# Performance work log

Measured on AMD Instinct MI355X. Metric: run time of the kernel, lower is better.

## Reference

```python
import jax, jax.numpy as jnp
import numpy as np

# BEV grid constants from init_kwargs (gen_dx_bx)
DX = jnp.array([0.3, 0.3, 20.0], dtype=jnp.float32)          # dx
BX_LO = jnp.array([-54.0, -54.0, -10.0], dtype=jnp.float32)  # bx - dx/2 = lower bound
NXX, NXY, NZ = 360, 360, 1                                    # nx = (360, 360, 1)


def setup_inputs() -> dict:
    key = jax.random.key(0)
    k1, k2, k3 = jax.random.split(key, 3)
    B, D, fH, fW, C = 4, 118, 32, 88, 80
    iH, iW = 256, 704
    x = jax.random.normal(k1, (B, D, fH, fW, C), dtype=jnp.float32)
    # frustum exactly as create_frustum(): (D, fH, fW, 3) with (u, v, depth)
    ds = jnp.arange(1.0, 60.0, 0.5, dtype=jnp.float32)[:, None, None] * jnp.ones((1, fH, fW), jnp.float32)
    xs = jnp.linspace(0.0, iW - 1.0, fW, dtype=jnp.float32)[None, None, :] * jnp.ones((D, fH, 1), jnp.float32)
    ys = jnp.linspace(0.0, iH - 1.0, fH, dtype=jnp.float32)[None, :, None] * jnp.ones((D, 1, fW), jnp.float32)
    frustum = jnp.stack([xs, ys, ds], axis=-1)
    # realistic pinhole intrinsics (well-conditioned for torch.inverse analog)
    fx = 560.0
    K = jnp.array([[fx, 0.0, (iW - 1) / 2.0], [0.0, fx, (iH - 1) / 2.0], [0.0, 0.0, 1.0]], dtype=jnp.float32)
    intrins = jnp.tile(K[None], (B, 1, 1))
    # camera->lidar: cam z -> lidar x, cam x -> -y, cam y -> -z, with small yaw jitter per sample
    Rbase = jnp.array([[0.0, 0.0, 1.0], [-1.0, 0.0, 0.0], [0.0, -1.0, 0.0]], dtype=jnp.float32)
    ang = jax.random.uniform(k2, (B,), minval=-0.2, maxval=0.2, dtype=jnp.float32)
    c, s = jnp.cos(ang), jnp.sin(ang)
    z0, o = jnp.zeros_like(c), jnp.ones_like(c)
    Ryaw = jnp.stack([jnp.stack([c, -s, z0], -1), jnp.stack([s, c, z0], -1), jnp.stack([z0, z0, o], -1)], axis=-2)
    rots = Ryaw @ Rbase[None]
    trans = jax.random.normal(k3, (B, 3), dtype=jnp.float32) * 0.5
    return {"x": x, "camera2lidar_rots": rots, "camera2lidar_trans": trans, "intrins": intrins, "frustum": frustum}


def reference(x, camera2lidar_rots, camera2lidar_trans, intrins, frustum):
    B, D, H, W, C = x.shape
    # --- get_geometry ---
    # unproject pixel (u,v,d) -> camera coords (u*d, v*d, d)
    pts = jnp.concatenate([frustum[..., :2] * frustum[..., 2:3], frustum[..., 2:3]], axis=-1)  # (D,H,W,3)
    combine = camera2lidar_rots @ jnp.linalg.inv(intrins)  # (B,3,3)
    geom = jnp.einsum('bij,dhwj->bdhwi', combine, pts) + camera2lidar_trans[:, None, None, None, :]  # (B,D,H,W,3)
    # --- bev_pool ---
    feats = x.reshape(-1, C)                                      # (Nprime, C)
    # torch .long() truncates toward zero -> numpy-style astype cast matches
    coords = ((geom - BX_LO) / DX).astype(jnp.int32).reshape(-1, 3)  # (Nprime, 3) voxel ix
    Np = feats.shape[0]
    batch_ix = jnp.repeat(jnp.arange(B, dtype=jnp.int32), Np // B)
    nx = jnp.array([NXX, NXY, NZ], dtype=jnp.int32)
    kept = jnp.all((coords >= 0) & (coords < nx), axis=-1)
    # linear voxel index ordered (b, z, x, y); out-of-range points go to a trash segment
    lin = ((batch_ix * NZ + coords[:, 2]) * NXX + coords[:, 0]) * NXY + coords[:, 1]
    nseg = B * NZ * NXX * NXY
    lin = jnp.where(kept, lin, nseg)
    pooled = jax.ops.segment_sum(feats, lin, num_segments=nseg + 1)[:-1]  # (B*Z*X*Y, C)
    out = pooled.reshape(B, NZ, NXX, NXY, C).transpose(0, 1, 4, 2, 3)     # (B, Z, C, X, Y)
    # torch: cat(unbind(dim=2 of (B,C,Z,X,Y)), dim=1) == (B, Z*C, X, Y) with Z-major blocks
    final = out.reshape(B, NZ * C, NXX, NXY)
    return final
```

## Files before the change

kernel.cpp:

```cpp
#include <hip/hip_runtime.h>
#include <hip/hip_bf16.h>

constexpr int B  = 4;
constexpr int D  = 118;
constexpr int FH = 32;
constexpr int FW = 88;
constexpr int C  = 80;
constexpr int NX = 360, NY = 360;
constexpr int XY = NX * NY;
constexpr int OUT_PER_B = C * XY;
constexpr int CELLS = B * XY;
constexpr int RPB = D * FW;
constexpr int CAP = 64;

constexpr int WPB = 16;
constexpr int NWB = (FW + WPB - 1) / WPB;
constexpr int K1_THREADS = WPB * (C / 4);

constexpr size_t CNT_BYTES    = (size_t)CELLS * 4;
constexpr size_t BUCKET_BYTES = (size_t)CELLS * CAP * 2;
constexpr size_t RAYFEAT_OFF  = CNT_BYTES + BUCKET_BYTES;


__global__ __launch_bounds__(K1_THREADS)
void ray_reduce_kernel(const float* __restrict__ x,
                       const float* __restrict__ rots,
                       const float* __restrict__ trans,
                       const float* __restrict__ intr,
                       const float* __restrict__ fr,
                       int* __restrict__ cnt,
                       unsigned short* __restrict__ bucket,
                       float* __restrict__ rayfeat) {
    const int g  = blockIdx.x;
    const int wg = g % NWB;
    const int bd = g / NWB;
    const int d  = bd % D;
    const int b  = bd / D;

    __shared__ int      sCell[WPB];
    __shared__ unsigned sMask[WPB];

    const int tid = threadIdx.x;

    if (tid < WPB) {
        const int w = wg * WPB + tid;
        int cell = -1;
        unsigned zmask = 0;
        if (w < FW) {
            const float* K = intr + b * 9;
            const float* R = rots + b * 9;
            const float i00 = 1.0f / K[0];
            const float i11 = 1.0f / K[4];
            const float i22 = 1.0f / K[8];
            const float i12 = -(K[5] * i22) / K[4];
            const float i01 = -(K[1] * i11) / K[0];
            const float i02 = -(fmaf(K[1], i12, K[2] * i22)) / K[0];
            const float inv[9] = { i00, i01, i02, 0.f, i11, i12, 0.f, 0.f, i22 };
            float cb[9];
            #pragma unroll
            for (int i = 0; i < 3; ++i) {
                #pragma unroll
                for (int j = 0; j < 3; ++j) {
                    float a = R[i * 3 + 0] * inv[0 * 3 + j];
                    a = fmaf(R[i * 3 + 1], inv[1 * 3 + j], a);
                    a = fmaf(R[i * 3 + 2], inv[2 * 3 + j], a);
                    cb[i * 3 + j] = a;
                }
            }
            const float tx = trans[b * 3 + 0];
            const float ty = trans[b * 3 + 1];
            const float tz = trans[b * 3 + 2];

            const float* frd = fr + (size_t)d * FH * FW * 3;
            const float dd = frd[2];
            const float u  = frd[w * 3 + 0];
            const float v0 = frd[1];

            const float p0 = u * dd;
            const float p2 = dd;
            const float p1_0 = v0 * dd;

            const float g0 = fmaf(cb[2], p2, fmaf(cb[1], p1_0, cb[0] * p0)) + tx;
            const float g1 = fmaf(cb[5], p2, fmaf(cb[4], p1_0, cb[3] * p0)) + ty;
            const int c0 = (int)((g0 + 54.0f) / 0.3f);
            const int c1 = (int)((g1 + 54.0f) / 0.3f);

            #pragma unroll
            for (int h = 0; h < FH; ++h) {
                const float vh = frd[h * FW * 3 + 1];
                const float p1h = vh * dd;
                const float g2 = fmaf(cb[8], p2, fmaf(cb[7], p1h, cb[6] * p0)) + tz;
                const int c2 = (int)((g2 + 10.0f) / 20.0f);
                if (c2 == 0) zmask |= (1u << h);
            }

            if (c0 >= 0 && c0 < NX && c1 >= 0 && c1 < NY && zmask != 0) {
                cell = b * XY + c0 * NY + c1;
            }
        }
        sCell[tid] = cell;
        sMask[tid] = zmask;
        if (cell >= 0) {
            const int rid = d * FW + w;
            const int idx = atomicAdd(&cnt[cell], 1);
            if (idx < CAP) bucket[(size_t)cell * CAP + idx] = (unsigned short)rid;
        }
    }
    __syncthreads();

    const int wl = tid / 20;
    const int q  = tid - wl * 20;
    const int w  = wg * WPB + wl;
    const int cell = sCell[wl];
    if (cell >= 0) {
        const unsigned zmask = sMask[wl];
        float4 acc = make_float4(0.f, 0.f, 0.f, 0.f);
        const float* xb = x + (((size_t)b * D + d) * FH) * (FW * C)
                            + (size_t)w * C + q * 4;
        #pragma unroll
        for (int h = 0; h < FH; ++h) {
            if ((zmask >> h) & 1u) {
                const float4 v = *(const float4*)(xb + (size_t)h * (FW * C));
                acc.x += v.x; acc.y += v.y; acc.z += v.z; acc.w += v.w;
            }
        }
        const size_t gray = (size_t)b * RPB + d * FW + w;
        *(float4*)(rayfeat + gray * C + q * 4) = acc;
    }
}

constexpr int GTH = 256;

__global__ __launch_bounds__(GTH)
void gather_kernel(const int* __restrict__ cnt,
                   const unsigned short* __restrict__ bucket,
                   const float* __restrict__ rayfeat,
                   float* __restrict__ out) {
    const int b    = blockIdx.y;
    const int flat = blockIdx.x * GTH + threadIdx.x;
    if (flat >= XY) return;
    const int cell = b * XY + flat;
    const int n = min(cnt[cell], CAP);
    const unsigned short* bk = bucket + (size_t)cell * CAP;
    float* ob = out + (size_t)b * OUT_PER_B + flat;

    #pragma unroll
    for (int ch = 0; ch < 4; ++ch) {
        float acc[20];
        #pragma unroll
        for (int j = 0; j < 20; ++j) acc[j] = 0.f;
        for (int i = 0; i < n; ++i) {
            const float* rf = rayfeat + ((size_t)b * RPB + bk[i]) * C + ch * 20;
            #pragma unroll
            for (int j5 = 0; j5 < 5; ++j5) {
                const float4 v = *(const float4*)(rf + j5 * 4);
                acc[j5 * 4 + 0] += v.x;
                acc[j5 * 4 + 1] += v.y;
                acc[j5 * 4 + 2] += v.z;
                acc[j5 * 4 + 3] += v.w;
            }
        }
        #pragma unroll
        for (int j = 0; j < 20; ++j) {
            ob[(size_t)(ch * 20 + j) * XY] = acc[j];
        }
    }
}

extern "C" void kernel_launch(void* const* d_in, const int* in_sizes, int n_in,
                              void* d_out, int out_size, void* d_ws, size_t ws_size,
                              hipStream_t stream) {
    const float* x     = (const float*)d_in[0];
    const float* rots  = (const float*)d_in[1];
    const float* trans = (const float*)d_in[2];
    const float* intr  = (const float*)d_in[3];
    const float* fr    = (const float*)d_in[4];
    float* out = (float*)d_out;

    int* cnt               = (int*)d_ws;
    unsigned short* bucket = (unsigned short*)((char*)d_ws + CNT_BYTES);
    float* rayfeat         = (float*)((char*)d_ws + RAYFEAT_OFF);

    hipMemsetAsync(cnt, 0, CNT_BYTES, stream);

    ray_reduce_kernel<<<B * D * NWB, K1_THREADS, 0, stream>>>(
        x, rots, trans, intr, fr, cnt, bucket, rayfeat);

    dim3 ggrid((XY + GTH - 1) / GTH, B);
    gather_kernel<<<ggrid, GTH, 0, stream>>>(cnt, bucket, rayfeat, out);
}
```

Baseline: 663.1 us.

## Replace bucket-and-gather pooling with direct atomic scatter into zeroed output

Drops the per-cell bucket lists, the intermediate per-ray feature buffer and the separate gather kernel. Each ray's height-reduced features are now atomically added straight into the output, which is zeroed with a memset beforehand. This removes one kernel launch, the count and bucket atomics, and a round trip of ray features through global memory. In exchange it adds scattered float atomics with a stride of one channel plane each, a full-output memset, and a summation order that is no longer deterministic.

```diff
diff --git a/kernel.cpp b/kernel.cpp
--- a/kernel.cpp
+++ b/kernel.cpp
@@ -1,5 +1,4 @@
 #include <hip/hip_runtime.h>
-#include <hip/hip_bf16.h>
 
 constexpr int B  = 4;
 constexpr int D  = 118;
@@ -9,42 +8,33 @@
 constexpr int NX = 360, NY = 360;
 constexpr int XY = NX * NY;
 constexpr int OUT_PER_B = C * XY;
-constexpr int CELLS = B * XY;
-constexpr int RPB = D * FW;
-constexpr int CAP = 64;
 
 constexpr int WPB = 16;
 constexpr int NWB = (FW + WPB - 1) / WPB;
 constexpr int K1_THREADS = WPB * (C / 4);
 
-constexpr size_t CNT_BYTES    = (size_t)CELLS * 4;
-constexpr size_t BUCKET_BYTES = (size_t)CELLS * CAP * 2;
-constexpr size_t RAYFEAT_OFF  = CNT_BYTES + BUCKET_BYTES;
-
 
 __global__ __launch_bounds__(K1_THREADS)
-void ray_reduce_kernel(const float* __restrict__ x,
-                       const float* __restrict__ rots,
-                       const float* __restrict__ trans,
-                       const float* __restrict__ intr,
-                       const float* __restrict__ fr,
-                       int* __restrict__ cnt,
-                       unsigned short* __restrict__ bucket,
-                       float* __restrict__ rayfeat) {
+void fused_scatter_kernel(const float* __restrict__ x,
+                          const float* __restrict__ rots,
+                          const float* __restrict__ trans,
+                          const float* __restrict__ intr,
+                          const float* __restrict__ fr,
+                          float* __restrict__ out) {
     const int g  = blockIdx.x;
     const int wg = g % NWB;
     const int bd = g / NWB;
     const int d  = bd % D;
     const int b  = bd / D;
 
-    __shared__ int      sCell[WPB];
+    __shared__ int      sFlat[WPB];
     __shared__ unsigned sMask[WPB];
 
     const int tid = threadIdx.x;
 
     if (tid < WPB) {
         const int w = wg * WPB + tid;
-        int cell = -1;
+        int flat = -1;
         unsigned zmask = 0;
         if (w < FW) {
             const float* K = intr + b * 9;
@@ -95,24 +85,19 @@
             }
 
             if (c0 >= 0 && c0 < NX && c1 >= 0 && c1 < NY && zmask != 0) {
-                cell = b * XY + c0 * NY + c1;
+                flat = c0 * NY + c1;
             }
         }
-        sCell[tid] = cell;
+        sFlat[tid] = flat;
         sMask[tid] = zmask;
-        if (cell >= 0) {
-            const int rid = d * FW + w;
-            const int idx = atomicAdd(&cnt[cell], 1);
-            if (idx < CAP) bucket[(size_t)cell * CAP + idx] = (unsigned short)rid;
-        }
     }
     __syncthreads();
 
     const int wl = tid / 20;
     const int q  = tid - wl * 20;
     const int w  = wg * WPB + wl;
-    const int cell = sCell[wl];
-    if (cell >= 0) {
+    const int flat = sFlat[wl];
+    if (flat >= 0) {
         const unsigned zmask = sMask[wl];
         float4 acc = make_float4(0.f, 0.f, 0.f, 0.f);
         const float* xb = x + (((size_t)b * D + d) * FH) * (FW * C)
@@ -124,46 +109,11 @@
                 acc.x += v.x; acc.y += v.y; acc.z += v.z; acc.w += v.w;
             }
         }
-        const size_t gray = (size_t)b * RPB + d * FW + w;
-        *(float4*)(rayfeat + gray * C + q * 4) = acc;
-    }
-}
-
-constexpr int GTH = 256;
-
-__global__ __launch_bounds__(GTH)
-void gather_kernel(const int* __restrict__ cnt,
-                   const unsigned short* __restrict__ bucket,
-                   const float* __restrict__ rayfeat,
-                   float* __restrict__ out) {
-    const int b    = blockIdx.y;
-    const int flat = blockIdx.x * GTH + threadIdx.x;
-    if (flat >= XY) return;
-    const int cell = b * XY + flat;
-    const int n = min(cnt[cell], CAP);
-    const unsigned short* bk = bucket + (size_t)cell * CAP;
-    float* ob = out + (size_t)b * OUT_PER_B + flat;
-
-    #pragma unroll
-    for (int ch = 0; ch < 4; ++ch) {
-        float acc[20];
-        #pragma unroll
-        for (int j = 0; j < 20; ++j) acc[j] = 0.f;
-        for (int i = 0; i < n; ++i) {
-            const float* rf = rayfeat + ((size_t)b * RPB + bk[i]) * C + ch * 20;
-            #pragma unroll
-            for (int j5 = 0; j5 < 5; ++j5) {
-                const float4 v = *(const float4*)(rf + j5 * 4);
-                acc[j5 * 4 + 0] += v.x;
-                acc[j5 * 4 + 1] += v.y;
-                acc[j5 * 4 + 2] += v.z;
-                acc[j5 * 4 + 3] += v.w;
-            }
-        }
-        #pragma unroll
-        for (int j = 0; j < 20; ++j) {
-            ob[(size_t)(ch * 20 + j) * XY] = acc[j];
-        }
+        float* ob = out + (size_t)b * OUT_PER_B + (size_t)(q * 4) * XY + flat;
+        atomicAdd(ob,                acc.x);
+        atomicAdd(ob + XY,           acc.y);
+        atomicAdd(ob + 2 * (size_t)XY, acc.z);
+        atomicAdd(ob + 3 * (size_t)XY, acc.w);
     }
 }
 
@@ -177,15 +127,8 @@
     const float* fr    = (const float*)d_in[4];
     float* out = (float*)d_out;
 
-    int* cnt               = (int*)d_ws;
-    unsigned short* bucket = (unsigned short*)((char*)d_ws + CNT_BYTES);
-    float* rayfeat         = (float*)((char*)d_ws + RAYFEAT_OFF);
+    hipMemsetAsync(out, 0, (size_t)out_size, stream);
 
-    hipMemsetAsync(cnt, 0, CNT_BYTES, stream);
-
-    ray_reduce_kernel<<<B * D * NWB, K1_THREADS, 0, stream>>>(
-        x, rots, trans, intr, fr, cnt, bucket, rayfeat);
-
-    dim3 ggrid((XY + GTH - 1) / GTH, B);
-    gather_kernel<<<ggrid, GTH, 0, stream>>>(cnt, bucket, rayfeat, out);
+    fused_scatter_kernel<<<B * D * NWB, K1_THREADS, 0, stream>>>(
+        x, rots, trans, intr, fr, out);
 }
```

Measured after the change: 661.4 us. Within noise of the previous version (-0.3%).
